# Optimization experiments

Hardware: AMD Instinct MI355X
Metric: run time of the kernel (lower is better)

The kernel has to match this reference:

```python
import jax, jax.numpy as jnp
import numpy as np
from math import log2, ceil

NUM_LEAVES = 128
KERNEL = 8
STRIDE = 8
PADDING = 0
LR = 0.3

LEAF_NUM = 2 ** ceil(log2(NUM_LEAVES))   # 128
DEPTH = int(log2(LEAF_NUM))              # 7
NUM_NODES = 2 * LEAF_NUM - 1             # 255


def _ancestor_table():
    # A[j-1, t-1] = global heap index of the ancestor of node j at tree level t,
    # or -1 if t exceeds j's own level. Nodes use heap indexing: children of i
    # are 2i+1, 2i+2 (matches the layer bookkeeping in the torch module).
    A = np.full((NUM_NODES - 1, DEPTH), -1, dtype=np.int32)
    for j in range(1, NUM_NODES):
        lvl = int(np.floor(np.log2(j + 1)))
        anc = j
        for t in range(lvl, 0, -1):
            A[j - 1, t - 1] = anc
            anc = (anc - 1) // 2
    return jnp.asarray(A)

_ANC = _ancestor_table()  # (NUM_NODES-1, DEPTH)


def img2patches(x):
    x = jnp.pad(x, PADDING)
    H, W = x.shape
    n0 = (H - KERNEL) // STRIDE + 1
    n1 = (W - KERNEL) // STRIDE + 1
    win = jnp.arange(KERNEL)
    rows = jnp.arange(n0)[:, None] * STRIDE + win[None, :]  # (n0, k)
    cols = jnp.arange(n1)[:, None] * STRIDE + win[None, :]  # (n1, k)
    p = x[rows[:, None, :, None], cols[None, :, None, :]]   # (n0, n1, k, k)
    return p.reshape(n0 * n1, KERNEL * KERNEL)


def setup_inputs() -> dict:
    key = jax.random.key(0)
    k1, k2 = jax.random.split(key)
    image = jax.random.uniform(k1, (2048, 2048), dtype=jnp.float32)
    nodes = jax.random.uniform(k2, (NUM_NODES, KERNEL * KERNEL), dtype=jnp.float32)
    return {"image": image, "nodes": nodes}


def reference(image, nodes):
    X = img2patches(image)                      # (P, k^2)
    P = X.shape[0]

    # --- hierarchical BMU descent (binary tree, DEPTH levels) ---
    cur = jnp.zeros((P,), dtype=jnp.int32)      # root
    bmu_levels = []
    for _ in range(DEPTH):
        c0 = 2 * cur + 1
        c1 = 2 * cur + 2
        # pnorm with p=2 in the source is (sum((a-b)^2))^2 -- monotone, kept faithful
        d0 = jnp.sum((nodes[c0] - X) ** 2, axis=-1) ** 2
        d1 = jnp.sum((nodes[c1] - X) ** 2, axis=-1) ** 2
        cur = jnp.where(d1 < d0, c1, c0)        # tie -> first (c0), like torch.min
        bmu_levels.append(cur)
    bmu_path = jnp.stack(bmu_levels, axis=1)    # (P, DEPTH), bmu at levels 1..DEPTH

    # --- layer_state for every non-root node: number of levels at which the
    # node's ancestor coincides with the BMU chain (== the torch concatenated
    # layer_state, columns ordered by global node index 1..NUM_NODES-1) ---
    state = jnp.sum(_ANC[None, :, :] == bmu_path[:, None, :], axis=-1)  # (P, N-1)

    lrates = LR * (2.0 ** jnp.arange(1, DEPTH + 2, dtype=jnp.float32)) / 2.0 ** (DEPTH + 1)
    lrs = lrates[state]                          # (P, N-1)

    # mean_p lrs[p,j] * (X[p,:] - nodes[1+j,:])
    #   = (lrs^T @ X)/P - mean_p(lrs)[:,None] * nodes[1:]
    upd = jnp.einsum('pj,pk->jk', lrs, X) / P - lrs.mean(axis=0)[:, None] * nodes[1:]
    new_nodes = nodes.at[1:].add(upd)

    return new_nodes, cur[:, None]               # updated codebook, leaf BMU per patch
```

## Files before the change

kernel.cpp:

```cpp
#include <hip/hip_runtime.h>

#define IMG_W 2048
#define NUM_NODES 255
#define NLEAF 128
#define DEPTH 7
#define RS 68

template<int CTRL>
__device__ __forceinline__ float dpp_add(float x) {
    int v = __builtin_amdgcn_update_dpp(0, __float_as_int(x), CTRL, 0xF, 0xF, true);
    return x + __int_as_float(v);
}
__device__ __forceinline__ float group16_sum(float x) {
    x = dpp_add<0xB1>(x);
    x = dpp_add<0x4E>(x);
    x = dpp_add<0x141>(x);
    x = dpp_add<0x128>(x);
    return x;
}

__global__ __launch_bounds__(1024, 8) void fusedK(const float* __restrict__ img,
                                                  const float* __restrict__ nodes,
                                                  float* __restrict__ leaf_out,
                                                  float* __restrict__ S,
                                                  unsigned* __restrict__ cnt)
{
    __shared__ float nds[NUM_NODES * RS];
    __shared__ unsigned cntl[NLEAF];
    float* Sl = nds;

    const int t = threadIdx.x;
    const int b = blockIdx.x;
    const int g = t >> 4;
    const int q = t & 15;
    const int q4 = q * 4;

    if (t < NLEAF) cntl[t] = 0u;

    const float4* ng = (const float4*)nodes;
    for (int i = t; i < NUM_NODES * 16; i += 1024) {
        *(float4*)&nds[(i >> 4) * RS + (i & 15) * 4] = ng[i];
    }

    float4 xv[2];
    int pid[2];
    #pragma unroll
    for (int ch = 0; ch < 2; ++ch) {
        const int p = b * 128 + ch * 64 + g;
        pid[ch] = p;
        const int r = p >> 8, c = p & 255;
        xv[ch] = *(const float4*)(img + (size_t)(r * 8 + (q >> 1)) * IMG_W + c * 8 + (q & 1) * 4);
    }
    __syncthreads();

    int leaf[2];
    #pragma unroll
    for (int ch = 0; ch < 2; ++ch) {
        const float4 x = xv[ch];
        int cur = 0;
        #pragma unroll
        for (int lvl = 0; lvl < DEPTH; ++lvl) {
            const int c0 = 2 * cur + 1;
            const float* base = &nds[c0 * RS + q4];
            const float4 a  = *(const float4*)(base);
            const float4 bb = *(const float4*)(base + RS);
            float s0 = 0.f, s1 = 0.f, d;
            d = a.x  - x.x; s0 = fmaf(d, d, s0);
            d = a.y  - x.y; s0 = fmaf(d, d, s0);
            d = a.z  - x.z; s0 = fmaf(d, d, s0);
            d = a.w  - x.w; s0 = fmaf(d, d, s0);
            d = bb.x - x.x; s1 = fmaf(d, d, s1);
            d = bb.y - x.y; s1 = fmaf(d, d, s1);
            d = bb.z - x.z; s1 = fmaf(d, d, s1);
            d = bb.w - x.w; s1 = fmaf(d, d, s1);
            s0 = group16_sum(s0);
            s1 = group16_sum(s1);
            cur = (s1 < s0) ? (c0 + 1) : c0;
        }
        leaf[ch] = cur;
        if (q == 0) leaf_out[pid[ch]] = (float)cur;
    }
    __syncthreads();

    for (int i = t; i < NLEAF * RS; i += 1024) Sl[i] = 0.0f;
    __syncthreads();

    #pragma unroll
    for (int ch = 0; ch < 2; ++ch) {
        const int L = leaf[ch] - 127;
        const float4 x = xv[ch];
        float* dst = &Sl[L * RS + q4];
        atomicAdd(dst + 0, x.x);
        atomicAdd(dst + 1, x.y);
        atomicAdd(dst + 2, x.z);
        atomicAdd(dst + 3, x.w);
        if (q == 0) atomicAdd(&cntl[L], 1u);
    }
    __syncthreads();

    for (int i = t; i < NLEAF * 64; i += 1024) {
        const float v = Sl[(i >> 6) * RS + (i & 63)];
        if (v != 0.0f) atomicAdd(&S[i], v);
    }
    if (t < NLEAF && cntl[t] != 0u) atomicAdd(&cnt[t], cntl[t]);
}

__global__ __launch_bounds__(256) void updateK(const float* __restrict__ nodes,
                                               const float* __restrict__ S,
                                               const unsigned* __restrict__ cnt,
                                               float* __restrict__ out)
{
    const int gid = blockIdx.x * 256 + threadIdx.x;
    if (gid >= NUM_NODES * 64) return;
    const int n = gid >> 6, k = gid & 63;
    const float nd = nodes[gid];
    if (n == 0) { out[gid] = nd; return; }

    const int pos = n + 1;
    const int Ln = 31 - __clz(pos);
    float su = 0.f, sc = 0.f;
    #pragma unroll 8
    for (int L = 0; L < NLEAF; ++L) {
        const int a = (128 + L) >> (7 - Ln);
        const int x = pos ^ a;
        const int state = (x == 0) ? Ln : (Ln - (31 - __clz(x)) - 1);
        const float lr = 0.3f * ((float)(1 << state) * (1.0f / 128.0f));
        su = fmaf(lr, S[L * 64 + k], su);
        sc = fmaf(lr, (float)cnt[L], sc);
    }
    const float invP = 1.0f / 65536.0f;
    out[gid] = nd + su * invP - (sc * invP) * nd;
}

extern "C" void kernel_launch(void* const* d_in, const int* in_sizes, int n_in,
                              void* d_out, int out_size, void* d_ws, size_t ws_size,
                              hipStream_t stream)
{
    const float* img   = (const float*)d_in[0];
    const float* nodes = (const float*)d_in[1];

    float* out_nodes = (float*)d_out;
    float* out_leaf  = out_nodes + NUM_NODES * 64;

    float*    S   = (float*)d_ws;
    unsigned* cnt = (unsigned*)(S + NLEAF * 64);

    hipMemsetAsync(d_ws, 0, (NLEAF * 64) * sizeof(float) + NLEAF * sizeof(unsigned), stream);
    fusedK<<<512, 1024, 0, stream>>>(img, nodes, out_leaf, S, cnt);
    updateK<<<64, 256, 0, stream>>>(nodes, S, cnt, out_nodes);
}
```

Before: 112.7 us.

## Split fused descent kernel into separate descent and accumulation kernels

Splits the fused kernel in two. A descent kernel uses 512-thread blocks and writes the leaf index per patch. A new accumulation kernel rereads the image and leaf indices, stages 256 patches per block in shared memory, and does LDS atomic accumulation with one thread per feature column. This cuts the number of blocks flushing partial sums to global memory from 512 to 256. In exchange it adds a kernel launch, reads the image a second time, and serialises the LDS atomic loop over 64 patches per wave.

```diff
diff --git a/kernel.cpp b/kernel.cpp
--- a/kernel.cpp
+++ b/kernel.cpp
@@ -19,15 +19,11 @@
     return x;
 }
 
-__global__ __launch_bounds__(1024, 8) void fusedK(const float* __restrict__ img,
-                                                  const float* __restrict__ nodes,
-                                                  float* __restrict__ leaf_out,
-                                                  float* __restrict__ S,
-                                                  unsigned* __restrict__ cnt)
+__global__ __launch_bounds__(512, 4) void descendK(const float* __restrict__ img,
+                                                   const float* __restrict__ nodes,
+                                                   float* __restrict__ leaf_out)
 {
     __shared__ float nds[NUM_NODES * RS];
-    __shared__ unsigned cntl[NLEAF];
-    float* Sl = nds;
 
     const int t = threadIdx.x;
     const int b = blockIdx.x;
@@ -35,25 +31,20 @@
     const int q = t & 15;
     const int q4 = q * 4;
 
-    if (t < NLEAF) cntl[t] = 0u;
-
     const float4* ng = (const float4*)nodes;
-    for (int i = t; i < NUM_NODES * 16; i += 1024) {
+    for (int i = t; i < NUM_NODES * 16; i += 512) {
         *(float4*)&nds[(i >> 4) * RS + (i & 15) * 4] = ng[i];
     }
 
     float4 xv[2];
-    int pid[2];
     #pragma unroll
     for (int ch = 0; ch < 2; ++ch) {
-        const int p = b * 128 + ch * 64 + g;
-        pid[ch] = p;
+        const int p = b * 64 + ch * 32 + g;
         const int r = p >> 8, c = p & 255;
         xv[ch] = *(const float4*)(img + (size_t)(r * 8 + (q >> 1)) * IMG_W + c * 8 + (q & 1) * 4);
     }
     __syncthreads();
 
-    int leaf[2];
     #pragma unroll
     for (int ch = 0; ch < 2; ++ch) {
         const float4 x = xv[ch];
@@ -77,28 +68,50 @@
             s1 = group16_sum(s1);
             cur = (s1 < s0) ? (c0 + 1) : c0;
         }
-        leaf[ch] = cur;
-        if (q == 0) leaf_out[pid[ch]] = (float)cur;
+        if (q == 0) leaf_out[b * 64 + ch * 32 + g] = (float)cur;
+    }
+}
+
+__global__ __launch_bounds__(256) void accumK(const float* __restrict__ img,
+                                              const float* __restrict__ leaf_out,
+                                              float* __restrict__ S,
+                                              unsigned* __restrict__ cnt)
+{
+    __shared__ float XN[256 * RS];
+    __shared__ float Sl[NLEAF * RS];
+    __shared__ int   Ll[256];
+    __shared__ unsigned cntl[NLEAF];
+
+    const int t = threadIdx.x;
+    const int b = blockIdx.x;
+    const int p = b * 256 + t;
+    const int r = p >> 8, c = p & 255;
+
+    for (int i = t; i < NLEAF * RS; i += 256) Sl[i] = 0.0f;
+    if (t < NLEAF) cntl[t] = 0u;
+
+    {
+        float* st = &XN[t * RS];
+        #pragma unroll
+        for (int ki = 0; ki < 8; ++ki) {
+            const float4* rowp = (const float4*)(img + (size_t)(r * 8 + ki) * IMG_W + c * 8);
+            *(float4*)&st[ki * 8]     = rowp[0];
+            *(float4*)&st[ki * 8 + 4] = rowp[1];
+        }
+    }
+    Ll[t] = (int)leaf_out[p] - 127;
+    __syncthreads();
+
+    const int w = t >> 6, k = t & 63;
+    for (int i = 0; i < 64; ++i) {
+        const int pl = w * 64 + i;
+        const int L  = Ll[pl];
+        atomicAdd(&Sl[L * RS + k], XN[pl * RS + k]);
+        if (k == 0) atomicAdd(&cntl[L], 1u);
     }
     __syncthreads();
 
-    for (int i = t; i < NLEAF * RS; i += 1024) Sl[i] = 0.0f;
-    __syncthreads();
-
-    #pragma unroll
-    for (int ch = 0; ch < 2; ++ch) {
-        const int L = leaf[ch] - 127;
-        const float4 x = xv[ch];
-        float* dst = &Sl[L * RS + q4];
-        atomicAdd(dst + 0, x.x);
-        atomicAdd(dst + 1, x.y);
-        atomicAdd(dst + 2, x.z);
-        atomicAdd(dst + 3, x.w);
-        if (q == 0) atomicAdd(&cntl[L], 1u);
-    }
-    __syncthreads();
-
-    for (int i = t; i < NLEAF * 64; i += 1024) {
+    for (int i = t; i < NLEAF * 64; i += 256) {
         const float v = Sl[(i >> 6) * RS + (i & 63)];
         if (v != 0.0f) atomicAdd(&S[i], v);
     }
@@ -146,6 +159,7 @@
     unsigned* cnt = (unsigned*)(S + NLEAF * 64);
 
     hipMemsetAsync(d_ws, 0, (NLEAF * 64) * sizeof(float) + NLEAF * sizeof(unsigned), stream);
-    fusedK<<<512, 1024, 0, stream>>>(img, nodes, out_leaf, S, cnt);
+    descendK<<<1024, 512, 0, stream>>>(img, nodes, out_leaf);
+    accumK<<<256, 256, 0, stream>>>(img, out_leaf, S, cnt);
     updateK<<<64, 256, 0, stream>>>(nodes, S, cnt, out_nodes);
 }
```

Measured after the change: 118.8 us. +5.4%, slower.

## Replace LDS atomic scatter with ballot-driven per-leaf gather reduction

Applied to the files above, without the earlier changes.

Instead of zeroing a shared leaf-sum table and scattering patch vectors into it with LDS float atomics, patches are stored in shared memory along with their leaf ids. Each wavefront then owns 8 leaf rows and uses ballots to find matching patches, summing them in registers. This removes the LDS zeroing pass and contended shared atomics, and only nonzero rows are flushed to global with atomics. The launch-bounds occupancy hint is also lowered from 8 to 4, which may change register allocation. The serial ballot loops could be uneven when many patches land in one leaf.

```diff
diff --git a/kernel.cpp b/kernel.cpp
--- a/kernel.cpp
+++ b/kernel.cpp
@@ -19,15 +19,15 @@
     return x;
 }
 
-__global__ __launch_bounds__(1024, 8) void fusedK(const float* __restrict__ img,
+__global__ __launch_bounds__(1024, 4) void fusedK(const float* __restrict__ img,
                                                   const float* __restrict__ nodes,
                                                   float* __restrict__ leaf_out,
                                                   float* __restrict__ S,
                                                   unsigned* __restrict__ cnt)
 {
     __shared__ float nds[NUM_NODES * RS];
-    __shared__ unsigned cntl[NLEAF];
-    float* Sl = nds;
+    __shared__ int Lbuf[128];
+    float* XN = nds;
 
     const int t = threadIdx.x;
     const int b = blockIdx.x;
@@ -35,25 +35,20 @@
     const int q = t & 15;
     const int q4 = q * 4;
 
-    if (t < NLEAF) cntl[t] = 0u;
-
     const float4* ng = (const float4*)nodes;
     for (int i = t; i < NUM_NODES * 16; i += 1024) {
         *(float4*)&nds[(i >> 4) * RS + (i & 15) * 4] = ng[i];
     }
 
     float4 xv[2];
-    int pid[2];
     #pragma unroll
     for (int ch = 0; ch < 2; ++ch) {
         const int p = b * 128 + ch * 64 + g;
-        pid[ch] = p;
         const int r = p >> 8, c = p & 255;
         xv[ch] = *(const float4*)(img + (size_t)(r * 8 + (q >> 1)) * IMG_W + c * 8 + (q & 1) * 4);
     }
     __syncthreads();
 
-    int leaf[2];
     #pragma unroll
     for (int ch = 0; ch < 2; ++ch) {
         const float4 x = xv[ch];
@@ -77,32 +72,50 @@
             s1 = group16_sum(s1);
             cur = (s1 < s0) ? (c0 + 1) : c0;
         }
-        leaf[ch] = cur;
-        if (q == 0) leaf_out[pid[ch]] = (float)cur;
+        if (q == 0) {
+            leaf_out[b * 128 + ch * 64 + g] = (float)cur;
+            Lbuf[ch * 64 + g] = cur - 127;
+        }
     }
-    __syncthreads();
-
-    for (int i = t; i < NLEAF * RS; i += 1024) Sl[i] = 0.0f;
     __syncthreads();
 
     #pragma unroll
     for (int ch = 0; ch < 2; ++ch) {
-        const int L = leaf[ch] - 127;
-        const float4 x = xv[ch];
-        float* dst = &Sl[L * RS + q4];
-        atomicAdd(dst + 0, x.x);
-        atomicAdd(dst + 1, x.y);
-        atomicAdd(dst + 2, x.z);
-        atomicAdd(dst + 3, x.w);
-        if (q == 0) atomicAdd(&cntl[L], 1u);
+        *(float4*)&XN[(ch * 64 + g) * RS + q4] = xv[ch];
     }
     __syncthreads();
 
-    for (int i = t; i < NLEAF * 64; i += 1024) {
-        const float v = Sl[(i >> 6) * RS + (i & 63)];
-        if (v != 0.0f) atomicAdd(&S[i], v);
+    const int w = t >> 6, k = t & 63;
+    const int L0 = Lbuf[k];
+    const int L1 = Lbuf[64 + k];
+    float acc[8];
+    int   cc[8];
+    #pragma unroll
+    for (int r = 0; r < 8; ++r) { acc[r] = 0.0f; cc[r] = 0; }
+
+    #pragma unroll
+    for (int r = 0; r < 8; ++r) {
+        const int row = w * 8 + r;
+        unsigned long long m0 = __ballot(L0 == row);
+        unsigned long long m1 = __ballot(L1 == row);
+        while (m0) {
+            const int p = __ffsll((unsigned long long)m0) - 1;  m0 &= m0 - 1;
+            acc[r] += XN[p * RS + k];  cc[r]++;
+        }
+        while (m1) {
+            const int p = 64 + __ffsll((unsigned long long)m1) - 1;  m1 &= m1 - 1;
+            acc[r] += XN[p * RS + k];  cc[r]++;
+        }
     }
-    if (t < NLEAF && cntl[t] != 0u) atomicAdd(&cnt[t], cntl[t]);
+
+    #pragma unroll
+    for (int r = 0; r < 8; ++r) {
+        if (cc[r] > 0) {
+            const int row = w * 8 + r;
+            atomicAdd(&S[row * 64 + k], acc[r]);
+            if (k == 0) atomicAdd(&cnt[row], (unsigned)cc[r]);
+        }
+    }
 }
 
 __global__ __launch_bounds__(256) void updateK(const float* __restrict__ nodes,
```

Measured after the change: 176.2 us. 56.4% more time.
